# Performance work log

Hardware: AMD Instinct MI355X
Metric: run time of the kernel (lower is better)

## Reference

```python
import jax, jax.numpy as jnp
import numpy as np

B, T, C = 2, 2048, 1024
H = 16
DK = C // H          # 64
BLOCK = 2049         # block_size; w2 has BLOCK-1 = 2048 columns
NEG = -1e10


def setup_inputs() -> dict:
    key = jax.random.key(0)
    ks = jax.random.split(key, 9)
    s = 1.0 / np.sqrt(C)
    return {
        "x":      jax.random.normal(ks[0], (B, T, C), jnp.float32),
        "w1_w":   jax.random.uniform(ks[1], (C, C), jnp.float32, -s, s),
        "w1_b":   jax.random.uniform(ks[2], (C,), jnp.float32, -s, s),
        "w2":     jax.random.uniform(ks[3], (DK, BLOCK - 1), jnp.float32, -0.001, 0.001),
        "b2":     jnp.zeros((BLOCK - 1,), jnp.float32),
        "val_w":  jax.random.uniform(ks[4], (C, C), jnp.float32, -s, s),
        "val_b":  jax.random.uniform(ks[5], (C,), jnp.float32, -s, s),
        "proj_w": jax.random.uniform(ks[6], (C, C), jnp.float32, -s, s),
        "proj_b": jax.random.uniform(ks[7], (C,), jnp.float32, -s, s),
    }


def reference(x, w1_w, w1_b, w2, b2, val_w, val_b, proj_w, proj_b):
    b, t, c = x.shape
    dk = c // H
    # relu(w1(x)) -> (B,H,T,dk); torch Linear: x @ W.T + b
    relu_out = jax.nn.relu(x @ w1_w.T + w1_b).reshape(b, t, H, dk).transpose(0, 2, 1, 3)
    v = (x @ val_w.T + val_b).reshape(b, t, H, dk).transpose(0, 2, 1, 3)
    # learned query-only scores: (B,H,T,BLOCK-1) -> slice to (B,H,T,T)
    scores = (jnp.einsum('bhtd,dk->bhtk', relu_out, w2) + b2)[:, :, :t, :t]
    causal = jnp.tril(jnp.ones((t, t), bool))
    scores = jnp.where(causal, scores, NEG)
    prob = jax.nn.softmax(scores, axis=-1)
    y = jnp.einsum('bhts,bhsd->bhtd', prob, v).transpose(0, 2, 1, 3).reshape(b, t, c)
    return y @ proj_w.T + proj_b
```

## Files before the change

kernel.cpp:

```cpp
#include <hip/hip_runtime.h>
#include <hip/hip_bf16.h>
#include <cstdint>
#include <cstddef>

#define BATCH 2
#define TDIM 2048
#define CDIM 1024
#define HN 16
#define DKD 64

typedef __attribute__((ext_vector_type(8))) short s8v;
typedef __attribute__((ext_vector_type(4))) short s4v;
typedef __attribute__((ext_vector_type(4))) float f4v;
typedef __attribute__((ext_vector_type(16))) float f16v;

__device__ __forceinline__ short f2bf(float f) {
  unsigned u = __float_as_uint(f);
  unsigned r = u + 0x7fffu + ((u >> 16) & 1u);
  return (short)(r >> 16);
}

__device__ __forceinline__ unsigned cvtpk_bf16(float lo, float hi) {
  unsigned r;
  asm("v_cvt_pk_bf16_f32 %0, %1, %2" : "=v"(r) : "v"(lo), "v"(hi));
  return r;
}

__device__ __forceinline__ void plswap(unsigned& a, unsigned& b) {
  asm volatile("v_permlane32_swap_b32 %0, %1" : "+v"(a), "+v"(b));
}

__device__ __forceinline__ f16v fzero16() {
  f16v z;
#pragma unroll
  for (int i = 0; i < 16; i++) z[i] = 0.f;
  return z;
}

#define GLDS16(g, l)                                                         \
  __builtin_amdgcn_global_load_lds(                                          \
      (const __attribute__((address_space(1))) unsigned*)(g),                \
      (__attribute__((address_space(3))) unsigned*)(l), 16, 0, 0)

__global__ void cvt4(const float* __restrict__ s, short* __restrict__ d, int n) {
  int i = (blockIdx.x * 256 + threadIdx.x) * 4;
  if (i >= n) return;
  const float4 v = *(const float4*)(s + i);
  s4v o;
  o[0] = f2bf(v.x); o[1] = f2bf(v.y); o[2] = f2bf(v.z); o[3] = f2bf(v.w);
  *(s4v*)(d + i) = o;
}

__global__ void w2frag(const float* __restrict__ s, short* __restrict__ d) {
  const int t = blockIdx.x;
  const int i = threadIdx.x >> 6;
  const int lane = threadIdx.x & 63;
  const int hi = lane >> 5, qr = lane & 31;
  union { short a[8]; s8v v; } o;
#pragma unroll
  for (int e = 0; e < 8; ++e)
    o.a[e] = f2bf(s[(size_t)(i * 16 + hi * 8 + e) * 2048 + t * 32 + qr]);
  *(s8v*)(d + ((size_t)(t * 4 + i) * 64 + lane) * 8) = o.v;
}

template <int MODE>
__global__ __launch_bounds__(256) void gemm_bt(
    const short* __restrict__ A, const short* __restrict__ Bw,
    const float* __restrict__ bias0, const float* __restrict__ bias1,
    short* __restrict__ out0, short* __restrict__ out1,
    float* __restrict__ outf, int M, int N, int K) {
  __shared__ __align__(16) short As[128 * 32];
  __shared__ __align__(16) short Bs[128 * 32];
  const int tid = threadIdx.x;
  const int w = tid >> 6, lane = tid & 63, lg = lane >> 4, lc = lane & 15;
  const int m0 = blockIdx.y * 128, n0 = blockIdx.x * 128;
  const int wr = w >> 1, wc = w & 1;

  f4v acc[4][4];
#pragma unroll
  for (int i = 0; i < 4; i++)
#pragma unroll
    for (int j = 0; j < 4; j++) acc[i][j] = (f4v){0.f, 0.f, 0.f, 0.f};

  for (int k0 = 0; k0 < K; k0 += 32) {
#pragma unroll
    for (int i = 0; i < 2; i++) {
      int off = i * 2048 + w * 512 + lane * 8;
      int row = off >> 5, col = off & 31;
      GLDS16(A + (size_t)(m0 + row) * K + k0 + col, &As[i * 2048 + w * 512]);
      GLDS16(Bw + (size_t)(n0 + row) * K + k0 + col, &Bs[i * 2048 + w * 512]);
    }
    __syncthreads();
    s8v af[4], bf[4];
#pragma unroll
    for (int mi = 0; mi < 4; mi++)
      af[mi] = *(const s8v*)&As[(wr * 64 + mi * 16 + lc) * 32 + lg * 8];
#pragma unroll
    for (int ni = 0; ni < 4; ni++)
      bf[ni] = *(const s8v*)&Bs[(wc * 64 + ni * 16 + lc) * 32 + lg * 8];
#pragma unroll
    for (int mi = 0; mi < 4; mi++)
#pragma unroll
      for (int ni = 0; ni < 4; ni++)
        acc[mi][ni] = __builtin_amdgcn_mfma_f32_16x16x32_bf16(
            af[mi], bf[ni], acc[mi][ni], 0, 0, 0);
    __syncthreads();
  }

#pragma unroll
  for (int mi = 0; mi < 4; mi++) {
#pragma unroll
    for (int ni = 0; ni < 4; ni++) {
      int col = n0 + wc * 64 + ni * 16 + lc;
#pragma unroll
      for (int r = 0; r < 4; r++) {
        int row = m0 + wr * 64 + mi * 16 + lg * 4 + r;
        float v = acc[mi][ni][r];
        if (MODE == 0) {
          int bidx = row >> 11, tg = row & 2047;
          if (col < CDIM) {
            v += bias0[col];
            v = fmaxf(v, 0.f);
            int bh = bidx * HN + (col >> 6);
            int d = col & 63;
            size_t idx = (((size_t)(bh * 64 + (tg >> 5)) * 4 + (d >> 4)) * 64 +
                          ((d >> 3) & 1) * 32 + (tg & 31)) * 8 + (d & 7);
            out0[idx] = f2bf(v);
          } else {
            int c2 = col - CDIM;
            v += bias1[c2];
            int bh = bidx * HN + (c2 >> 6);
            int d = c2 & 63;
            int k = tg;
            size_t idx = (((size_t)(bh * 64 + (k >> 5)) * 4 + (d >> 5) * 2 +
                           ((k >> 4) & 1)) * 64 + ((k >> 3) & 1) * 32 + (d & 31)) * 8 +
                         (k & 7);
            out1[idx] = f2bf(v);
          }
        } else {
          v += bias0[col];
          outf[(size_t)row * N + col] = v;
        }
      }
    }
  }
}

__global__ __launch_bounds__(256, 4) void attn(
    const short* __restrict__ RQ2, const short* __restrict__ VT2,
    const short* __restrict__ W2T2, const float* __restrict__ b2,
    short* __restrict__ Y) {
  __shared__ float Olds[4 * 32 * 65];
  __shared__ float llds[256];
  const int tid = threadIdx.x;
  const int w = tid >> 6, lane = tid & 63;
  const int qr = lane & 31, hi = lane >> 5;
  const int bh = blockIdx.x;
  const int qt = gridDim.y - 1 - blockIdx.y;
  const int b = bh >> 4, h = bh & 15;
  const int q0 = qt * 32;
  const int nt = qt + 1;

  const short* Rp = RQ2 + ((size_t)(bh * 64 + qt) * 4) * 512 + lane * 8;
  s8v rq[4];
#pragma unroll
  for (int i = 0; i < 4; ++i) rq[i] = *(const s8v*)(Rp + i * 512);

  const short* Vb = VT2 + (size_t)bh * 64 * 2048;

  f16v o0 = fzero16(), o1 = fzero16();
  float lpart = 0.f;

  for (int t = w; t < nt; t += 4) {
    const short* wp = W2T2 + (size_t)t * 2048 + lane * 8;
    s8v wf[4];
#pragma unroll
    for (int i = 0; i < 4; ++i) wf[i] = *(const s8v*)(wp + i * 512);
    const short* vp = Vb + (size_t)t * 2048 + lane * 8;
    s8v vf[4];
#pragma unroll
    for (int i = 0; i < 4; ++i) vf[i] = *(const s8v*)(vp + i * 512);
    float4 bb[4];
#pragma unroll
    for (int j = 0; j < 4; ++j)
      bb[j] = *(const float4*)(b2 + t * 32 + 4 * hi + 8 * j);

    f16v sacc = fzero16();
#pragma unroll
    for (int i = 0; i < 4; ++i)
      sacc = __builtin_amdgcn_mfma_f32_32x32x16_bf16(wf[i], rq[i], sacc, 0, 0, 0);

    float pv[16];
#pragma unroll
    for (int j = 0; j < 4; ++j) {
      pv[4 * j + 0] = sacc[4 * j + 0] + bb[j].x;
      pv[4 * j + 1] = sacc[4 * j + 1] + bb[j].y;
      pv[4 * j + 2] = sacc[4 * j + 2] + bb[j].z;
      pv[4 * j + 3] = sacc[4 * j + 3] + bb[j].w;
    }
    if (t == nt - 1) {
#pragma unroll
      for (int r = 0; r < 16; ++r) {
        int kl = (r & 3) + 8 * (r >> 2) + 4 * hi;
        if (kl > qr) pv[r] = -1e10f;
      }
    }
#pragma unroll
    for (int r = 0; r < 16; ++r) pv[r] = __expf(pv[r]);
    {
      float t0 = pv[0] + pv[1], t1 = pv[2] + pv[3];
      float t2 = pv[4] + pv[5], t3 = pv[6] + pv[7];
      float t4 = pv[8] + pv[9], t5 = pv[10] + pv[11];
      float t6 = pv[12] + pv[13], t7 = pv[14] + pv[15];
      lpart += ((t0 + t1) + (t2 + t3)) + ((t4 + t5) + (t6 + t7));
    }

    unsigned c[8];
#pragma unroll
    for (int j = 0; j < 8; ++j) c[j] = cvtpk_bf16(pv[2 * j], pv[2 * j + 1]);
    plswap(c[0], c[2]);
    plswap(c[1], c[3]);
    plswap(c[4], c[6]);
    plswap(c[5], c[7]);
    union { unsigned u[4]; s8v v; } pa0, pa1;
    pa0.u[0] = c[0]; pa0.u[1] = c[1]; pa0.u[2] = c[2]; pa0.u[3] = c[3];
    pa1.u[0] = c[4]; pa1.u[1] = c[5]; pa1.u[2] = c[6]; pa1.u[3] = c[7];

    o0 = __builtin_amdgcn_mfma_f32_32x32x16_bf16(pa0.v, vf[0], o0, 0, 0, 0);
    o0 = __builtin_amdgcn_mfma_f32_32x32x16_bf16(pa1.v, vf[1], o0, 0, 0, 0);
    o1 = __builtin_amdgcn_mfma_f32_32x32x16_bf16(pa0.v, vf[2], o1, 0, 0, 0);
    o1 = __builtin_amdgcn_mfma_f32_32x32x16_bf16(pa1.v, vf[3], o1, 0, 0, 0);
  }

#pragma unroll
  for (int r = 0; r < 16; ++r) {
    int ql = (r & 3) + 8 * (r >> 2) + 4 * hi;
    Olds[(w * 32 + ql) * 65 + qr] = o0[r];
    Olds[(w * 32 + ql) * 65 + 32 + qr] = o1[r];
  }
  llds[w * 64 + lane] = lpart;
  __syncthreads();

  const int q = tid >> 3;
  const int d0 = (tid & 7) * 8;
  float L = 0.f;
#pragma unroll
  for (int w4 = 0; w4 < 4; ++w4)
    L += llds[w4 * 64 + q] + llds[w4 * 64 + 32 + q];
  const float inv = 1.0f / L;
  union { short a[8]; s8v v; } yv;
#pragma unroll
  for (int j = 0; j < 8; ++j) {
    float acc = 0.f;
#pragma unroll
    for (int w4 = 0; w4 < 4; ++w4) acc += Olds[(w4 * 32 + q) * 65 + d0 + j];
    yv.a[j] = f2bf(acc * inv);
  }
  *(s8v*)(Y + ((size_t)b * TDIM + q0 + q) * CDIM + h * DKD + d0) = yv.v;
}

extern "C" void kernel_launch(void* const* d_in, const int* in_sizes, int n_in,
                              void* d_out, int out_size, void* d_ws, size_t ws_size,
                              hipStream_t stream) {
  const float* x     = (const float*)d_in[0];
  const float* w1w   = (const float*)d_in[1];
  const float* w1b   = (const float*)d_in[2];
  const float* w2    = (const float*)d_in[3];
  const float* b2    = (const float*)d_in[4];
  const float* valw  = (const float*)d_in[5];
  const float* valb  = (const float*)d_in[6];
  const float* projw = (const float*)d_in[7];
  const float* projb = (const float*)d_in[8];

  char* ws = (char*)d_ws;
  short* xb  = (short*)(ws);
  short* wb  = (short*)(ws + (8u << 20));
  short* pj  = (short*)(ws + (12u << 20));
  short* w2t = (short*)(ws + (14u << 20));
  short* Rb  = (short*)(ws + (16u << 20));
  short* Vt  = (short*)(ws + (24u << 20));
  short* Yb  = (short*)(ws + (32u << 20));

  cvt4<<<4096, 256, 0, stream>>>(x, xb, 4194304);
  cvt4<<<1024, 256, 0, stream>>>(w1w, wb, 1048576);
  cvt4<<<1024, 256, 0, stream>>>(valw, wb + 1048576, 1048576);
  cvt4<<<1024, 256, 0, stream>>>(projw, pj, 1048576);
  w2frag<<<64, 256, 0, stream>>>(w2, w2t);

  gemm_bt<0><<<dim3(16, 32), 256, 0, stream>>>(xb, wb, w1b, valb, Rb, Vt,
                                               nullptr, 4096, 2048, 1024);
  attn<<<dim3(32, 64), 256, 0, stream>>>(Rb, Vt, w2t, b2, Yb);
  gemm_bt<1><<<dim3(8, 32), 256, 0, stream>>>(Yb, pj, projb, nullptr, nullptr,
                                              nullptr, (float*)d_out, 4096,
                                              1024, 1024);
}
```

Before: 192.0 us.

## Fuse conversion kernels into one launch and double GEMM K-tile depth

Merges the four fp32-to-bf16 conversion launches and the w2 fragment-packing launch into a single prep kernel that dispatches on block index, removing four kernel launches and the gaps between them. The GEMM K step grows from 32 to 64, so each barrier pair covers two MFMA sub-steps, which halves the synchronisation count per output tile. The cost is doubled LDS per block and a row stride of 64 shorts that may add LDS bank conflicts.

```diff
diff --git a/kernel.cpp b/kernel.cpp
--- a/kernel.cpp
+++ b/kernel.cpp
@@ -42,25 +42,41 @@
       (const __attribute__((address_space(1))) unsigned*)(g),                \
       (__attribute__((address_space(3))) unsigned*)(l), 16, 0, 0)
 
-__global__ void cvt4(const float* __restrict__ s, short* __restrict__ d, int n) {
-  int i = (blockIdx.x * 256 + threadIdx.x) * 4;
-  if (i >= n) return;
+__device__ __forceinline__ void cvt_body(const float* __restrict__ s,
+                                         short* __restrict__ d, int bid) {
+  int i = (bid * 256 + (int)threadIdx.x) * 4;
   const float4 v = *(const float4*)(s + i);
   s4v o;
   o[0] = f2bf(v.x); o[1] = f2bf(v.y); o[2] = f2bf(v.z); o[3] = f2bf(v.w);
   *(s4v*)(d + i) = o;
 }
 
-__global__ void w2frag(const float* __restrict__ s, short* __restrict__ d) {
-  const int t = blockIdx.x;
-  const int i = threadIdx.x >> 6;
-  const int lane = threadIdx.x & 63;
-  const int hi = lane >> 5, qr = lane & 31;
-  union { short a[8]; s8v v; } o;
-#pragma unroll
-  for (int e = 0; e < 8; ++e)
-    o.a[e] = f2bf(s[(size_t)(i * 16 + hi * 8 + e) * 2048 + t * 32 + qr]);
-  *(s8v*)(d + ((size_t)(t * 4 + i) * 64 + lane) * 8) = o.v;
+__global__ __launch_bounds__(256) void prep(
+    const float* __restrict__ x, short* __restrict__ xb,
+    const float* __restrict__ w1w, const float* __restrict__ valw,
+    short* __restrict__ wb, const float* __restrict__ projw,
+    short* __restrict__ pj, const float* __restrict__ w2,
+    short* __restrict__ w2t) {
+  const int bid = blockIdx.x;
+  if (bid < 4096) {
+    cvt_body(x, xb, bid);
+  } else if (bid < 5120) {
+    cvt_body(w1w, wb, bid - 4096);
+  } else if (bid < 6144) {
+    cvt_body(valw, wb + 1048576, bid - 5120);
+  } else if (bid < 7168) {
+    cvt_body(projw, pj, bid - 6144);
+  } else {
+    const int t = bid - 7168;
+    const int i = threadIdx.x >> 6;
+    const int lane = threadIdx.x & 63;
+    const int hi = lane >> 5, qr = lane & 31;
+    union { short a[8]; s8v v; } o;
+#pragma unroll
+    for (int e = 0; e < 8; ++e)
+      o.a[e] = f2bf(w2[(size_t)(i * 16 + hi * 8 + e) * 2048 + t * 32 + qr]);
+    *(s8v*)(w2t + ((size_t)(t * 4 + i) * 64 + lane) * 8) = o.v;
+  }
 }
 
 template <int MODE>
@@ -69,8 +85,8 @@
     const float* __restrict__ bias0, const float* __restrict__ bias1,
     short* __restrict__ out0, short* __restrict__ out1,
     float* __restrict__ outf, int M, int N, int K) {
-  __shared__ __align__(16) short As[128 * 32];
-  __shared__ __align__(16) short Bs[128 * 32];
+  __shared__ __align__(16) short As[128 * 64];
+  __shared__ __align__(16) short Bs[128 * 64];
   const int tid = threadIdx.x;
   const int w = tid >> 6, lane = tid & 63, lg = lane >> 4, lc = lane & 15;
   const int m0 = blockIdx.y * 128, n0 = blockIdx.x * 128;
@@ -82,28 +98,31 @@
 #pragma unroll
     for (int j = 0; j < 4; j++) acc[i][j] = (f4v){0.f, 0.f, 0.f, 0.f};
 
-  for (int k0 = 0; k0 < K; k0 += 32) {
-#pragma unroll
-    for (int i = 0; i < 2; i++) {
+  for (int k0 = 0; k0 < K; k0 += 64) {
+#pragma unroll
+    for (int i = 0; i < 4; i++) {
       int off = i * 2048 + w * 512 + lane * 8;
-      int row = off >> 5, col = off & 31;
+      int row = off >> 6, col = off & 63;
       GLDS16(A + (size_t)(m0 + row) * K + k0 + col, &As[i * 2048 + w * 512]);
       GLDS16(Bw + (size_t)(n0 + row) * K + k0 + col, &Bs[i * 2048 + w * 512]);
     }
     __syncthreads();
-    s8v af[4], bf[4];
-#pragma unroll
-    for (int mi = 0; mi < 4; mi++)
-      af[mi] = *(const s8v*)&As[(wr * 64 + mi * 16 + lc) * 32 + lg * 8];
-#pragma unroll
-    for (int ni = 0; ni < 4; ni++)
-      bf[ni] = *(const s8v*)&Bs[(wc * 64 + ni * 16 + lc) * 32 + lg * 8];
-#pragma unroll
-    for (int mi = 0; mi < 4; mi++)
+#pragma unroll
+    for (int kk = 0; kk < 2; ++kk) {
+      s8v af[4], bf[4];
+#pragma unroll
+      for (int mi = 0; mi < 4; mi++)
+        af[mi] = *(const s8v*)&As[(wr * 64 + mi * 16 + lc) * 64 + kk * 32 + lg * 8];
 #pragma unroll
       for (int ni = 0; ni < 4; ni++)
-        acc[mi][ni] = __builtin_amdgcn_mfma_f32_16x16x32_bf16(
-            af[mi], bf[ni], acc[mi][ni], 0, 0, 0);
+        bf[ni] = *(const s8v*)&Bs[(wc * 64 + ni * 16 + lc) * 64 + kk * 32 + lg * 8];
+#pragma unroll
+      for (int mi = 0; mi < 4; mi++)
+#pragma unroll
+        for (int ni = 0; ni < 4; ni++)
+          acc[mi][ni] = __builtin_amdgcn_mfma_f32_16x16x32_bf16(
+              af[mi], bf[ni], acc[mi][ni], 0, 0, 0);
+    }
     __syncthreads();
   }
 
@@ -281,11 +300,7 @@
   short* Vt  = (short*)(ws + (24u << 20));
   short* Yb  = (short*)(ws + (32u << 20));
 
-  cvt4<<<4096, 256, 0, stream>>>(x, xb, 4194304);
-  cvt4<<<1024, 256, 0, stream>>>(w1w, wb, 1048576);
-  cvt4<<<1024, 256, 0, stream>>>(valw, wb + 1048576, 1048576);
-  cvt4<<<1024, 256, 0, stream>>>(projw, pj, 1048576);
-  w2frag<<<64, 256, 0, stream>>>(w2, w2t);
+  prep<<<7232, 256, 0, stream>>>(x, xb, w1w, valw, wb, projw, pj, w2, w2t);
 
   gemm_bt<0><<<dim3(16, 32), 256, 0, stream>>>(xb, wb, w1b, valb, Rb, Vt,
                                                nullptr, 4096, 2048, 1024);
```

New measurement: 182.0 us. 5.2% less time.
